# Performance work log

Hardware: AMD Instinct MI355X
Metric: run time of the kernel (lower is better)

The kernel has to match this reference:

```python
import jax, jax.numpy as jnp
import numpy as np

B, T, V, C, H, HS, L, DFF = 8192, 8, 65, 512, 8, 64, 6, 2048
LN_EPS = 1e-5


def _layernorm(x, g, b):
    mu = jnp.mean(x, axis=-1, keepdims=True)
    var = jnp.mean(jnp.square(x - mu), axis=-1, keepdims=True)
    return (x - mu) * jax.lax.rsqrt(var + LN_EPS) * g + b


def setup_inputs() -> dict:
    key = jax.random.key(0)
    ks = jax.random.split(key, 16)
    s = 0.02
    inp = {
        "idx": jax.random.randint(ks[0], (B, T), 0, V),
        "tok_table": jax.random.normal(ks[1], (V, C), jnp.float32) * s,
        "pos_table": jax.random.normal(ks[2], (T, C), jnp.float32) * s,
        "wq": jax.random.normal(ks[3], (L, H, C, HS), jnp.float32) * s,
        "wk": jax.random.normal(ks[4], (L, H, C, HS), jnp.float32) * s,
        "wv": jax.random.normal(ks[5], (L, H, C, HS), jnp.float32) * s,
        "proj_w": jax.random.normal(ks[6], (L, C, C), jnp.float32) * s,
        "proj_b": jnp.zeros((L, C), jnp.float32),
        "w1": jax.random.normal(ks[7], (L, C, DFF), jnp.float32) * s,
        "b1": jnp.zeros((L, DFF), jnp.float32),
        "w2": jax.random.normal(ks[8], (L, DFF, C), jnp.float32) * s,
        "b2": jnp.zeros((L, C), jnp.float32),
        "ln1_g": jnp.ones((L, C), jnp.float32),
        "ln1_b": jnp.zeros((L, C), jnp.float32),
        "ln2_g": jnp.ones((L, C), jnp.float32),
        "ln2_b": jnp.zeros((L, C), jnp.float32),
        "lm_w": jax.random.normal(ks[9], (C, V), jnp.float32) * s,
        "lm_b": jnp.zeros((V,), jnp.float32),
    }
    return inp


def reference(idx, tok_table, pos_table, wq, wk, wv, proj_w, proj_b,
              w1, b1, w2, b2, ln1_g, ln1_b, ln2_g, ln2_b, lm_w, lm_b):
    idx = idx[:, -T:]
    x = tok_table[idx] + pos_table[None, :T, :]  # [B,T,C]
    mask = jnp.tril(jnp.ones((T, T), bool))
    scale = C ** (-0.5)  # NOTE: original scales by n_embed, not head_size
    for l in range(L):
        q = jnp.einsum('btc,hcd->bhtd', x, wq[l])
        k = jnp.einsum('btc,hcd->bhtd', x, wk[l])
        v = jnp.einsum('btc,hcd->bhtd', x, wv[l])
        att = jnp.einsum('bhtd,bhsd->bhts', q, k) * scale
        att = jnp.where(mask, att, -jnp.inf)
        att = jax.nn.softmax(att, axis=-1)
        o = jnp.einsum('bhts,bhsd->bhtd', att, v)
        o = o.transpose(0, 2, 1, 3).reshape(x.shape[0], T, C)  # concat heads
        o = o @ proj_w[l] + proj_b[l]
        x = _layernorm(x + o, ln1_g[l], ln1_b[l])  # post-norm
        h = jax.nn.relu(x @ w1[l] + b1[l]) @ w2[l] + b2[l]
        x = _layernorm(x + h, ln2_g[l], ln2_b[l])
    logits = x @ lm_w + lm_b  # [B,T,V]
    return logits
```

## Files before the change

### kernel.cpp

```cpp
#include <hip/hip_runtime.h>
#include <hip/hip_bf16.h>
#include <math.h>

#define NTOK  65536
#define CDIM  512
#define NHEAD 8
#define HSZ   64
#define NLAYER 6
#define DFF   2048
#define VOCAB 65

typedef unsigned short u16;
typedef __attribute__((ext_vector_type(8))) __bf16 bf16x8;
typedef __attribute__((ext_vector_type(4))) float f32x4;
typedef __attribute__((ext_vector_type(8))) unsigned short ushort8;

__device__ __forceinline__ float b2f(u16 u) {
    union { unsigned int i; float f; } x; x.i = ((unsigned int)u) << 16; return x.f;
}
__device__ __forceinline__ u16 f2b(float f) {
    union { float f; unsigned int i; } x; x.f = f;
    unsigned int r = x.i + 0x7fffu + ((x.i >> 16) & 1u);
    return (u16)(r >> 16);
}

__device__ __forceinline__ void async16(const u16* g, u16* l) {
    __builtin_amdgcn_global_load_lds(
        (const __attribute__((address_space(1))) void*)g,
        (__attribute__((address_space(3))) void*)l, 16, 0, 0);
}

template<int JB, int IB>
__device__ __forceinline__ void mfma_quad(f32x4 (&acc)[4][8],
                                          const bf16x8 (&af)[4][2],
                                          const bf16x8 (&bf)[4][2])
{
#pragma unroll
    for (int kk = 0; kk < 2; kk++)
#pragma unroll
        for (int j = 0; j < 2; j++)
#pragma unroll
            for (int i = 0; i < 4; i++)
                acc[JB + j][IB + i] = __builtin_amdgcn_mfma_f32_16x16x32_bf16(
                    bf[JB + j][kk], af[i][kk], acc[JB + j][IB + i], 0, 0, 0);
}

template<int EPI>
__global__ __launch_bounds__(512, 2)
void gemm256(const u16* __restrict__ A, const u16* __restrict__ Bt,
             void* Cout, const float* __restrict__ bias,
             const u16* res, int K, int lda, int N, int tpb)
{
    extern __shared__ __attribute__((aligned(16))) u16 lds[];
    const int tid = threadIdx.x;
    const int bid = blockIdx.x;

    const int per_x = gridDim.x >> 4;
    const int xcd = bid & 7, wblk = bid >> 3;
    const int mt = xcd * per_x + (wblk >> 1);
    const int q  = wblk & 1;
    const int m0 = mt * 256;
    const int nt0 = q * tpb;

    const int lane = tid & 63, wvv = tid >> 6;
    const int wvm = wvv >> 2, wvn = wvv & 3;
    const int r16 = lane & 15, quad = lane >> 4;
    const int gk0 = quad ^ (r16 & 7);
    const int g0x8 = gk0 * 8, g1x8 = (gk0 ^ 4) * 8;
    const int arow = wvm * 128 + r16;
    const int brow = wvn * 64 + r16;

    const int srow = tid >> 3;
    const int sg = (tid & 7) ^ (srow & 7);
    const u16* pA  = A  + (size_t)(m0 + srow) * lda + sg * 8;
    const u16* pB0 = Bt + (size_t)(nt0 * 256 + srow) * K + sg * 8;
    u16* const ldst = lds + tid * 8;
    const size_t ldaq = (size_t)64 * lda, ldah = (size_t)128 * lda;
    const size_t kq = (size_t)64 * K, kh = (size_t)128 * K;
    const size_t bstride = (size_t)256 * K;

    const int nk = K >> 6;

    f32x4 acc[4][8];
    bf16x8 af[4][2], bf[4][2];

#define STAGE_A(c, kt, h) do { \
    async16(pA + ((h) ? ldah : 0) + (size_t)((kt) * 64),        ldst + (c) * 32768 + (h) * 8192); \
    async16(pA + ((h) ? ldah : 0) + ldaq + (size_t)((kt) * 64), ldst + (c) * 32768 + (h) * 8192 + 4096); } while (0)
#define STAGE_B(c, pb, kt, h) do { \
    async16((pb) + ((h) ? kh : 0) + (size_t)((kt) * 64),        ldst + (c) * 32768 + 16384 + (h) * 8192); \
    async16((pb) + ((h) ? kh : 0) + kq + (size_t)((kt) * 64),   ldst + (c) * 32768 + 16384 + (h) * 8192 + 4096); } while (0)
#define LD_A4(IB0) do { _Pragma("unroll") \
    for (int i = 0; i < 4; i++) { \
        const int ro = cb + (arow + ((IB0) + i) * 16) * 64; \
        af[i][0] = *(const bf16x8*)(const void*)&lds[ro + g0x8]; \
        af[i][1] = *(const bf16x8*)(const void*)&lds[ro + g1x8]; \
    } } while (0)
#define LD_B2(JB0) do { _Pragma("unroll") \
    for (int j = 0; j < 2; j++) { \
        const int ro = cb + 16384 + (brow + ((JB0) + j) * 16) * 64; \
        bf[(JB0) + j][0] = *(const bf16x8*)(const void*)&lds[ro + g0x8]; \
        bf[(JB0) + j][1] = *(const bf16x8*)(const void*)&lds[ro + g1x8]; \
    } } while (0)
#define LGKM0() do { asm volatile("s_waitcnt lgkmcnt(0)" ::: "memory"); \
                     __builtin_amdgcn_sched_barrier(0); } while (0)

    STAGE_A(0, 0, 0); STAGE_A(0, 0, 1);
    STAGE_B(0, pB0, 0, 0); STAGE_B(0, pB0, 0, 1);
    if (nk > 1) {
        STAGE_B(1, pB0, 1, 0); STAGE_B(1, pB0, 1, 1);
        asm volatile("s_waitcnt vmcnt(4)" ::: "memory");
    } else {
        asm volatile("s_waitcnt vmcnt(0)" ::: "memory");
    }
    __builtin_amdgcn_s_barrier();

    for (int j = 0; j < tpb; ++j) {
#pragma unroll
        for (int jj = 0; jj < 4; jj++)
#pragma unroll
            for (int ii = 0; ii < 8; ii++)
                acc[jj][ii] = (f32x4){0.f, 0.f, 0.f, 0.f};

        for (int t = 0; t < nk; ++t) {
            const int c = t & 1;
            const int cb = c * 32768;
            const bool haveA = !((j == tpb - 1) && (t == nk - 1));
            const int kta = (t + 1 < nk) ? (t + 1) : 0;
            int t2 = t + 2, j2 = j;
            if (t2 >= nk) { t2 -= nk; j2++; }
            const bool haveB = (j2 < tpb);
            const u16* pB2 = pB0 + (size_t)j2 * bstride;

            LD_A4(0);
            LD_B2(0);
            if (haveA) STAGE_A(c ^ 1, kta, 0);
            __builtin_amdgcn_s_barrier();
            LGKM0();
            __builtin_amdgcn_s_setprio(1);
            mfma_quad<0, 0>(acc, af, bf);
            __builtin_amdgcn_s_setprio(0);
            __builtin_amdgcn_s_barrier();

            LD_B2(2);
            if (haveA) STAGE_A(c ^ 1, kta, 1);
            __builtin_amdgcn_s_barrier();
            LGKM0();
            __builtin_amdgcn_s_setprio(1);
            mfma_quad<2, 0>(acc, af, bf);
            __builtin_amdgcn_s_setprio(0);
            __builtin_amdgcn_s_barrier();

            LD_A4(4);
            if (haveB) STAGE_B(c, pB2, t2, 0);
            __builtin_amdgcn_s_barrier();
            LGKM0();
            __builtin_amdgcn_s_setprio(1);
            mfma_quad<0, 4>(acc, af, bf);
            __builtin_amdgcn_s_setprio(0);
            __builtin_amdgcn_s_barrier();

            if (haveB) {
                STAGE_B(c, pB2, t2, 1);
                asm volatile("s_waitcnt vmcnt(4)" ::: "memory");
            } else {
                asm volatile("s_waitcnt vmcnt(0)" ::: "memory");
            }
            __builtin_amdgcn_s_barrier();
            __builtin_amdgcn_s_setprio(1);
            mfma_quad<2, 4>(acc, af, bf);
            __builtin_amdgcn_s_setprio(0);
            __builtin_amdgcn_s_barrier();
        }

        const int n0 = (nt0 + j) * 256;
#pragma unroll
        for (int i = 0; i < 8; i++) {
            const int row = m0 + wvm * 128 + i * 16 + r16;
#pragma unroll
            for (int jc = 0; jc < 4; jc++) {
                const int colb = n0 + wvn * 64 + jc * 16 + quad * 4;
                float v[4];
#pragma unroll
                for (int r = 0; r < 4; r++) v[r] = acc[jc][i][r];
                if (EPI == 1 || EPI == 2) {
                    const f32x4 b4 = *(const f32x4*)(const void*)&bias[colb];
#pragma unroll
                    for (int r = 0; r < 4; r++) v[r] += b4[r];
                }
                if (EPI == 1) {
                    const uint2 rv = *(const uint2*)(const void*)&res[(size_t)row * N + colb];
                    v[0] += b2f((u16)(rv.x & 0xffffu));
                    v[1] += b2f((u16)(rv.x >> 16));
                    v[2] += b2f((u16)(rv.y & 0xffffu));
                    v[3] += b2f((u16)(rv.y >> 16));
                }
                if (EPI == 2) {
#pragma unroll
                    for (int r = 0; r < 4; r++) v[r] = fmaxf(v[r], 0.f);
                }
                uint2 o;
                o.x = (unsigned)f2b(v[0]) | ((unsigned)f2b(v[1]) << 16);
                o.y = (unsigned)f2b(v[2]) | ((unsigned)f2b(v[3]) << 16);
                *(uint2*)(void*)&((u16*)Cout)[(size_t)row * N + colb] = o;
            }
        }
    }
#undef STAGE_A
#undef STAGE_B
#undef LD_A4
#undef LD_B2
#undef LGKM0
}

template<int EPI>
__global__ __launch_bounds__(512)
void gemm_bt(const u16* __restrict__ A, const u16* __restrict__ Bt,
             void* __restrict__ Cout, const float* __restrict__ bias,
             const u16* __restrict__ res, int K, int lda, int N, int Nout)
{
    __shared__ u16 lA[2 * 256 * 32];
    __shared__ u16 lB[2 * 128 * 32];
    const int tid  = threadIdx.x;

    const int Nx = gridDim.x;
    const int id = blockIdx.y * Nx + blockIdx.x;
    const int xcd = id & 7;
    const int j0  = id >> 3;
    const int mt  = xcd + 8 * (j0 / Nx);
    const int nt  = j0 - (j0 / Nx) * Nx;
    const int m0  = mt * 256;
    const int n0  = nt * 128;

    const int lane = tid & 63;
    const int wv   = tid >> 6;
    const int wr   = (wv >> 1) * 64;
    const int wc   = (wv & 1) * 64;
    const int r16  = lane & 15;
    const int quad = lane >> 4;

    f32x4 acc[4][4] = {};

    const int srow = tid >> 2, skseg = (tid & 3) * 8;
    const u16* pA  = A  + (size_t)(m0 + srow) * lda + skseg;
    const u16* pA2 = pA + (size_t)128 * lda;
    const u16* pB  = Bt + (size_t)(n0 + srow) * K + skseg;
    u16* lAt = &lA[(size_t)tid * 8];
    u16* lBt = &lB[(size_t)tid * 8];

    for (int k0 = 0; k0 < K; k0 += 64) {
        async16(pA  + k0,      lAt);
        async16(pA2 + k0,      lAt + 4096);
        async16(pA  + k0 + 32, lAt + 8192);
        async16(pA2 + k0 + 32, lAt + 12288);
        async16(pB  + k0,      lBt);
        async16(pB  + k0 + 32, lBt + 4096);
        __syncthreads();

#pragma unroll
        for (int s = 0; s < 2; s++) {
            const u16* bA = &lA[s * 8192];
            const u16* bB = &lB[s * 4096];
            bf16x8 af[4], bfr[4];
#pragma unroll
            for (int i = 0; i < 4; i++)
                af[i] = *(const bf16x8*)(const void*)&bA[(wr + i * 16 + r16) * 32 + quad * 8];
#pragma unroll
            for (int j = 0; j < 4; j++)
                bfr[j] = *(const bf16x8*)(const void*)&bB[(wc + j * 16 + r16) * 32 + quad * 8];
#pragma unroll
            for (int j = 0; j < 4; j++)
#pragma unroll
                for (int i = 0; i < 4; i++)
                    acc[j][i] = __builtin_amdgcn_mfma_f32_16x16x32_bf16(bfr[j], af[i], acc[j][i], 0, 0, 0);
        }
        __syncthreads();
    }

#pragma unroll
    for (int i = 0; i < 4; i++) {
        const int row = m0 + wr + i * 16 + r16;
#pragma unroll
        for (int j = 0; j < 4; j++) {
            const int colb = n0 + wc + j * 16 + quad * 4;
            float v[4];
#pragma unroll
            for (int r = 0; r < 4; r++) v[r] = acc[j][i][r];
            if (EPI == 3) {
#pragma unroll
                for (int r = 0; r < 4; r++) {
                    const int col = colb + r;
                    if (col < Nout)
                        ((float*)Cout)[(size_t)row * Nout + col] = v[r] + bias[col];
                }
            } else {
                uint2 o;
                o.x = (unsigned)f2b(v[0]) | ((unsigned)f2b(v[1]) << 16);
                o.y = (unsigned)f2b(v[2]) | ((unsigned)f2b(v[3]) << 16);
                *(uint2*)(void*)&((u16*)Cout)[(size_t)row * N + colb] = o;
            }
        }
    }
}

__global__ __launch_bounds__(256)
void attn_k(u16* __restrict__ qkv)
{
    __shared__ float sq[4][8][65], sk[4][8][65], sv[4][8][65], sp[4][64];
    const int w = threadIdx.x >> 6, lane = threadIdx.x & 63;
    const int unit = blockIdx.x * 4 + w;
    const int b = unit >> 3, h = unit & 7;
    const size_t base = (size_t)b * 8 * 1536 + h * 64;
    {
        const int t = lane >> 3, d0 = (lane & 7) * 8;
        const ushort8 q8 = *(const ushort8*)(const void*)&qkv[base + t * 1536 + d0];
        const ushort8 k8 = *(const ushort8*)(const void*)&qkv[base + t * 1536 + 512 + d0];
        const ushort8 v8 = *(const ushort8*)(const void*)&qkv[base + t * 1536 + 1024 + d0];
#pragma unroll
        for (int i = 0; i < 8; i++) {
            sq[w][t][d0 + i] = b2f(q8[i]);
            sk[w][t][d0 + i] = b2f(k8[i]);
            sv[w][t][d0 + i] = b2f(v8[i]);
        }
    }
    __syncthreads();
    const int t = lane >> 3, s = lane & 7;
    float sc = -1e30f;
    if (s <= t) {
        float d = 0.f;
#pragma unroll
        for (int c = 0; c < 64; c++) d += sq[w][t][c] * sk[w][s][c];
        sc = d * 0.04419417382415922f;
    }
    float mx = sc;
#pragma unroll
    for (int m = 1; m < 8; m <<= 1) mx = fmaxf(mx, __shfl_xor(mx, m, 8));
    float e = __expf(sc - mx);
    if (s > t) e = 0.f;
    float sum = e;
#pragma unroll
    for (int m = 1; m < 8; m <<= 1) sum += __shfl_xor(sum, m, 8);
    sp[w][lane] = e / sum;
    __syncthreads();
    {
        const int tt = lane >> 3, d0 = (lane & 7) * 8;
        float a[8] = {};
#pragma unroll
        for (int ss = 0; ss < 8; ss++) {
            const float p = sp[w][tt * 8 + ss];
#pragma unroll
            for (int i = 0; i < 8; i++) a[i] += p * sv[w][ss][d0 + i];
        }
        ushort8 o;
#pragma unroll
        for (int i = 0; i < 8; i++) o[i] = f2b(a[i]);
        *(ushort8*)(void*)&qkv[base + tt * 1536 + d0] = o;
    }
}

__global__ __launch_bounds__(256)
void ln_k(const u16* __restrict__ y, const float* __restrict__ g,
          const float* __restrict__ be, u16* __restrict__ x)
{
    const int w = threadIdx.x >> 6, lane = threadIdx.x & 63;
    const size_t tok = (size_t)blockIdx.x * 4 + w;
    const u16* row = y + tok * 512 + lane * 8;
    ushort8 raw = *(const ushort8*)(const void*)row;
    float v[8];
#pragma unroll
    for (int i = 0; i < 8; i++) v[i] = b2f(raw[i]);
    float s = 0.f;
#pragma unroll
    for (int i = 0; i < 8; i++) s += v[i];
#pragma unroll
    for (int m = 1; m < 64; m <<= 1) s += __shfl_xor(s, m, 64);
    const float mu = s * (1.f / 512.f);
    float q = 0.f;
#pragma unroll
    for (int i = 0; i < 8; i++) { float d = v[i] - mu; q += d * d; }
#pragma unroll
    for (int m = 1; m < 64; m <<= 1) q += __shfl_xor(q, m, 64);
    const float inv = rsqrtf(q * (1.f / 512.f) + 1e-5f);
    f32x4 g0  = *(const f32x4*)(const void*)&g[lane * 8];
    f32x4 g1  = *(const f32x4*)(const void*)&g[lane * 8 + 4];
    f32x4 b0  = *(const f32x4*)(const void*)&be[lane * 8];
    f32x4 b1v = *(const f32x4*)(const void*)&be[lane * 8 + 4];
    ushort8 o;
#pragma unroll
    for (int i = 0; i < 4; i++) o[i]     = f2b((v[i] - mu) * inv * g0[i] + b0[i]);
#pragma unroll
    for (int i = 0; i < 4; i++) o[i + 4] = f2b((v[i + 4] - mu) * inv * g1[i] + b1v[i]);
    *(ushort8*)(void*)&x[tok * 512 + lane * 8] = o;
}

__global__ __launch_bounds__(256)
void embed_k(const int* __restrict__ idx, const float* __restrict__ tokt,
             const float* __restrict__ pos, u16* __restrict__ xb)
{
    const int gid = blockIdx.x * 256 + threadIdx.x;
    const int tk = gid >> 6, seg = (gid & 63) * 8;
    const int t = tk & 7;
    const int ix = idx[tk];
    const f32x4 a0 = *(const f32x4*)(const void*)&tokt[(size_t)ix * 512 + seg];
    const f32x4 a1 = *(const f32x4*)(const void*)&tokt[(size_t)ix * 512 + seg + 4];
    const f32x4 p0 = *(const f32x4*)(const void*)&pos[t * 512 + seg];
    const f32x4 p1 = *(const f32x4*)(const void*)&pos[t * 512 + seg + 4];
    ushort8 o;
#pragma unroll
    for (int i = 0; i < 4; i++) o[i]     = f2b(a0[i] + p0[i]);
#pragma unroll
    for (int i = 0; i < 4; i++) o[i + 4] = f2b(a1[i] + p1[i]);
    *(ushort8*)(void*)&xb[(size_t)tk * 512 + seg] = o;
}

__global__ __launch_bounds__(256)
void conv_t2_k(const float* __restrict__ in, u16* __restrict__ out, int K, int N)
{
    __shared__ float t[32][33];
    const int tx = threadIdx.x & 31, ty4 = (threadIdx.x >> 5) * 4;
    const int n0 = blockIdx.x * 32, k0 = blockIdx.y * 32, l = blockIdx.z;
    const size_t per = (size_t)K * N;
    const float* src = in + l * per;
#pragma unroll
    for (int r = 0; r < 4; r++)
        t[ty4 + r][tx] = src[(size_t)(k0 + ty4 + r) * N + n0 + tx];
    __syncthreads();
    u16* dst = out + l * per;
#pragma unroll
    for (int r = 0; r < 4; r++)
        dst[(size_t)(n0 + ty4 + r) * K + k0 + tx] = f2b(t[tx][ty4 + r]);
}

__global__ __launch_bounds__(256)
void conv_qkv2_k(const float* __restrict__ wq, const float* __restrict__ wk,
                 const float* __restrict__ wv, u16* __restrict__ out)
{
    __shared__ float t[32][33];
    const int tx = threadIdx.x & 31, ty4 = (threadIdx.x >> 5) * 4;
    const int c0 = blockIdx.x * 32, d0 = blockIdx.y * 32;
    const int z = blockIdx.z;
    const int sel = z / 48, rem = z - sel * 48;
    const int l = rem >> 3, h = rem & 7;
    const float* src = (sel == 0) ? wq : (sel == 1) ? wk : wv;
    const float* sb = src + (((size_t)l * 8 + h) * 512) * 64;
#pragma unroll
    for (int r = 0; r < 4; r++)
        t[ty4 + r][tx] = sb[(size_t)(c0 + ty4 + r) * 64 + d0 + tx];
    __syncthreads();
    u16* dst = out + (size_t)l * 786432 + (size_t)(sel * 512 + h * 64 + d0) * 512;
#pragma unroll
    for (int r = 0; r < 4; r++)
        dst[(size_t)(ty4 + r) * 512 + c0 + tx] = f2b(t[tx][ty4 + r]);
}

__global__ __launch_bounds__(256)
void conv_lm_k(const float* __restrict__ lm_w, u16* __restrict__ out)
{
    int gid = blockIdx.x * 256 + threadIdx.x;
    int n = gid >> 9, c = gid & 511;
    out[gid] = (n < VOCAB) ? f2b(lm_w[(size_t)c * VOCAB + n]) : (u16)0;
}

extern "C" void kernel_launch(void* const* d_in, const int* in_sizes, int n_in,
                              void* d_out, int out_size, void* d_ws, size_t ws_size,
                              hipStream_t stream)
{
    const int*   idx    = (const int*)  d_in[0];
    const float* tokt   = (const float*)d_in[1];
    const float* post   = (const float*)d_in[2];
    const float* wq     = (const float*)d_in[3];
    const float* wk     = (const float*)d_in[4];
    const float* wvp    = (const float*)d_in[5];
    const float* proj_w = (const float*)d_in[6];
    const float* proj_b = (const float*)d_in[7];
    const float* w1     = (const float*)d_in[8];
    const float* b1     = (const float*)d_in[9];
    const float* w2     = (const float*)d_in[10];
    const float* b2     = (const float*)d_in[11];
    const float* ln1_g  = (const float*)d_in[12];
    const float* ln1_b  = (const float*)d_in[13];
    const float* ln2_g  = (const float*)d_in[14];
    const float* ln2_b  = (const float*)d_in[15];
    const float* lm_w   = (const float*)d_in[16];
    const float* lm_b   = (const float*)d_in[17];
    float* out = (float*)d_out;

    static int smem_set = 0;
    if (!smem_set) {
        smem_set = 1;
        hipFuncSetAttribute(reinterpret_cast<const void*>(&gemm256<0>),
                            hipFuncAttributeMaxDynamicSharedMemorySize, 131072);
        hipFuncSetAttribute(reinterpret_cast<const void*>(&gemm256<1>),
                            hipFuncAttributeMaxDynamicSharedMemorySize, 131072);
        hipFuncSetAttribute(reinterpret_cast<const void*>(&gemm256<2>),
                            hipFuncAttributeMaxDynamicSharedMemorySize, 131072);
    }

    char* ws = (char*)d_ws;
    u16* wqkvt = (u16*)(ws + 0);
    u16* wprjt = (u16*)(ws + 9437184);
    u16* ww1t  = (u16*)(ws + 12582912);
    u16* ww2t  = (u16*)(ws + 25165824);
    u16* wlmt  = (u16*)(ws + 37748736);
    u16* xb    = (u16*)(ws + 37879808);
    char* big  = ws + 104988672;

    const size_t fixed_bytes = 104988672ull;
    const size_t avail = (ws_size > fixed_bytes) ? (ws_size - fixed_bytes) : 0;
    int chunk_a = 8192, chunk_m = 8192;
    const int cands[3] = {65536, 32768, 16384};
    for (int i = 0; i < 3; i++)
        if ((size_t)cands[i] * 3072ull <= avail) { chunk_a = cands[i]; break; }
    for (int i = 0; i < 3; i++)
        if ((size_t)cands[i] * 4096ull <= avail) { chunk_m = cands[i]; break; }
    const int nca = NTOK / chunk_a, ncm = NTOK / chunk_m;
    u16* qkvc = (u16*)big;
    u16* h1c  = (u16*)big;

    conv_qkv2_k<<<dim3(16, 2, 144), 256, 0, stream>>>(wq, wk, wvp, wqkvt);
    conv_t2_k  <<<dim3(16, 16, 6), 256, 0, stream>>>(proj_w, wprjt, 512, 512);
    conv_t2_k  <<<dim3(64, 16, 6), 256, 0, stream>>>(w1, ww1t, 512, 2048);
    conv_t2_k  <<<dim3(16, 64, 6), 256, 0, stream>>>(w2, ww2t, 2048, 512);
    conv_lm_k  <<<128 * 512 / 256, 256, 0, stream>>>(lm_w, wlmt);

    embed_k<<<NTOK * 64 / 256, 256, 0, stream>>>(idx, tokt, post, xb);

    for (int l = 0; l < NLAYER; l++) {
        for (int c = 0; c < nca; c++) {
            const size_t t0 = (size_t)c * chunk_a;
            const int grid = (chunk_a / 256) * 2;
            gemm256<0><<<dim3(grid), 512, 131072, stream>>>(
                xb + t0 * 512, wqkvt + (size_t)l * 786432, qkvc,
                nullptr, nullptr, 512, 512, 1536, 3);
            attn_k<<<chunk_a / 4, 256, 0, stream>>>(qkvc);
            gemm256<1><<<dim3(grid), 512, 131072, stream>>>(
                qkvc, wprjt + (size_t)l * 262144, xb + t0 * 512,
                proj_b + l * 512, xb + t0 * 512, 512, 1536, 512, 1);
        }
        ln_k<<<NTOK / 4, 256, 0, stream>>>(xb, ln1_g + l * 512, ln1_b + l * 512, xb);
        for (int c = 0; c < ncm; c++) {
            const size_t t0 = (size_t)c * chunk_m;
            const int grid = (chunk_m / 256) * 2;
            gemm256<2><<<dim3(grid), 512, 131072, stream>>>(
                xb + t0 * 512, ww1t + (size_t)l * 1048576, h1c,
                b1 + l * 2048, nullptr, 512, 512, 2048, 4);
            gemm256<1><<<dim3(grid), 512, 131072, stream>>>(
                h1c, ww2t + (size_t)l * 1048576, xb + t0 * 512,
                b2 + l * 512, xb + t0 * 512, 2048, 2048, 512, 1);
        }
        ln_k<<<NTOK / 4, 256, 0, stream>>>(xb, ln2_g + l * 512, ln2_b + l * 512, xb);
    }

    gemm_bt<3><<<dim3(1, 256), 512, 0, stream>>>(
        xb, wlmt, out, lm_b, nullptr, 512, 512, 128, VOCAB);
}
```

Measured before the change: 4.151 ms.

## Specialize GEMM dimensions as template constants and simplify to single-barrier double buffering

The GEMM kernel now takes K, LDA, N and tiles-per-block as template parameters, so strides and trip counts are compile-time constants and the k-loop can be unrolled. The hand-interleaved four-phase schedule is replaced by a plain double buffer. That schedule split A/B staging across sub-steps, prefetched B two tiles ahead and used several barriers with lgkmcnt waits. The new loop issues all next-tile async loads up front, runs all MFMAs, then waits vmcnt(0) and takes one barrier. This removes barrier and wait overhead per k-step, but it shortens the prefetch distance and hides less memory latency behind compute.

Measured after the change: 5.257 ms. 26.7% more time.

```diff
diff --git a/kernel.cpp b/kernel.cpp
--- a/kernel.cpp
+++ b/kernel.cpp
@@ -45,13 +45,14 @@
                     bf[JB + j][kk], af[i][kk], acc[JB + j][IB + i], 0, 0, 0);
 }
 
-template<int EPI>
+template<int EPI, int K, int LDA, int N, int TPB>
 __global__ __launch_bounds__(512, 2)
 void gemm256(const u16* __restrict__ A, const u16* __restrict__ Bt,
-             void* Cout, const float* __restrict__ bias,
-             const u16* res, int K, int lda, int N, int tpb)
+             void* Cout, const float* __restrict__ bias, const u16* res)
 {
     extern __shared__ __attribute__((aligned(16))) u16 lds[];
+    constexpr int NK = K >> 6;
+    constexpr size_t BSTRIDE = (size_t)256 * K;
     const int tid = threadIdx.x;
     const int bid = blockIdx.x;
 
@@ -60,7 +61,7 @@
     const int mt = xcd * per_x + (wblk >> 1);
     const int q  = wblk & 1;
     const int m0 = mt * 256;
-    const int nt0 = q * tpb;
+    const int nt0 = q * TPB;
 
     const int lane = tid & 63, wvv = tid >> 6;
     const int wvm = wvv >> 2, wvn = wvv & 3;
@@ -72,14 +73,11 @@
 
     const int srow = tid >> 3;
     const int sg = (tid & 7) ^ (srow & 7);
-    const u16* pA  = A  + (size_t)(m0 + srow) * lda + sg * 8;
+    const u16* pA  = A  + (size_t)(m0 + srow) * LDA + sg * 8;
     const u16* pB0 = Bt + (size_t)(nt0 * 256 + srow) * K + sg * 8;
     u16* const ldst = lds + tid * 8;
-    const size_t ldaq = (size_t)64 * lda, ldah = (size_t)128 * lda;
-    const size_t kq = (size_t)64 * K, kh = (size_t)128 * K;
-    const size_t bstride = (size_t)256 * K;
-
-    const int nk = K >> 6;
+    constexpr size_t ldaq = (size_t)64 * LDA, ldah = (size_t)128 * LDA;
+    constexpr size_t kq = (size_t)64 * K, kh = (size_t)128 * K;
 
     f32x4 acc[4][8];
     bf16x8 af[4][2], bf[4][2];
@@ -102,74 +100,42 @@
         bf[(JB0) + j][0] = *(const bf16x8*)(const void*)&lds[ro + g0x8]; \
         bf[(JB0) + j][1] = *(const bf16x8*)(const void*)&lds[ro + g1x8]; \
     } } while (0)
-#define LGKM0() do { asm volatile("s_waitcnt lgkmcnt(0)" ::: "memory"); \
-                     __builtin_amdgcn_sched_barrier(0); } while (0)
 
     STAGE_A(0, 0, 0); STAGE_A(0, 0, 1);
     STAGE_B(0, pB0, 0, 0); STAGE_B(0, pB0, 0, 1);
-    if (nk > 1) {
-        STAGE_B(1, pB0, 1, 0); STAGE_B(1, pB0, 1, 1);
-        asm volatile("s_waitcnt vmcnt(4)" ::: "memory");
-    } else {
-        asm volatile("s_waitcnt vmcnt(0)" ::: "memory");
-    }
+    asm volatile("s_waitcnt vmcnt(0)" ::: "memory");
     __builtin_amdgcn_s_barrier();
 
-    for (int j = 0; j < tpb; ++j) {
+    for (int j = 0; j < TPB; ++j) {
+        const u16* pBj = pB0 + (size_t)j * BSTRIDE;
 #pragma unroll
         for (int jj = 0; jj < 4; jj++)
 #pragma unroll
             for (int ii = 0; ii < 8; ii++)
                 acc[jj][ii] = (f32x4){0.f, 0.f, 0.f, 0.f};
 
-        for (int t = 0; t < nk; ++t) {
+#pragma unroll 4
+        for (int t = 0; t < NK; ++t) {
             const int c = t & 1;
             const int cb = c * 32768;
-            const bool haveA = !((j == tpb - 1) && (t == nk - 1));
-            const int kta = (t + 1 < nk) ? (t + 1) : 0;
-            int t2 = t + 2, j2 = j;
-            if (t2 >= nk) { t2 -= nk; j2++; }
-            const bool haveB = (j2 < tpb);
-            const u16* pB2 = pB0 + (size_t)j2 * bstride;
-
-            LD_A4(0);
-            LD_B2(0);
-            if (haveA) STAGE_A(c ^ 1, kta, 0);
-            __builtin_amdgcn_s_barrier();
-            LGKM0();
+            if (t + 1 < NK) {
+                STAGE_A(c ^ 1, t + 1, 0); STAGE_A(c ^ 1, t + 1, 1);
+                STAGE_B(c ^ 1, pBj, t + 1, 0); STAGE_B(c ^ 1, pBj, t + 1, 1);
+            } else if (j + 1 < TPB) {
+                STAGE_A(c ^ 1, 0, 0); STAGE_A(c ^ 1, 0, 1);
+                STAGE_B(c ^ 1, pBj + BSTRIDE, 0, 0); STAGE_B(c ^ 1, pBj + BSTRIDE, 0, 1);
+            }
+            LD_A4(0); LD_B2(0); LD_B2(2);
             __builtin_amdgcn_s_setprio(1);
             mfma_quad<0, 0>(acc, af, bf);
-            __builtin_amdgcn_s_setprio(0);
-            __builtin_amdgcn_s_barrier();
-
-            LD_B2(2);
-            if (haveA) STAGE_A(c ^ 1, kta, 1);
-            __builtin_amdgcn_s_barrier();
-            LGKM0();
-            __builtin_amdgcn_s_setprio(1);
             mfma_quad<2, 0>(acc, af, bf);
             __builtin_amdgcn_s_setprio(0);
-            __builtin_amdgcn_s_barrier();
-
             LD_A4(4);
-            if (haveB) STAGE_B(c, pB2, t2, 0);
-            __builtin_amdgcn_s_barrier();
-            LGKM0();
             __builtin_amdgcn_s_setprio(1);
             mfma_quad<0, 4>(acc, af, bf);
-            __builtin_amdgcn_s_setprio(0);
-            __builtin_amdgcn_s_barrier();
-
-            if (haveB) {
-                STAGE_B(c, pB2, t2, 1);
-                asm volatile("s_waitcnt vmcnt(4)" ::: "memory");
-            } else {
-                asm volatile("s_waitcnt vmcnt(0)" ::: "memory");
-            }
-            __builtin_amdgcn_s_barrier();
-            __builtin_amdgcn_s_setprio(1);
             mfma_quad<2, 4>(acc, af, bf);
             __builtin_amdgcn_s_setprio(0);
+            asm volatile("s_waitcnt vmcnt(0)" ::: "memory");
             __builtin_amdgcn_s_barrier();
         }
 
@@ -210,7 +176,6 @@
 #undef STAGE_B
 #undef LD_A4
 #undef LD_B2
-#undef LGKM0
 }
 
 template<int EPI>
@@ -488,11 +453,13 @@
     static int smem_set = 0;
     if (!smem_set) {
         smem_set = 1;
-        hipFuncSetAttribute(reinterpret_cast<const void*>(&gemm256<0>),
+        hipFuncSetAttribute(reinterpret_cast<const void*>(&gemm256<0, 512, 512, 1536, 3>),
                             hipFuncAttributeMaxDynamicSharedMemorySize, 131072);
-        hipFuncSetAttribute(reinterpret_cast<const void*>(&gemm256<1>),
+        hipFuncSetAttribute(reinterpret_cast<const void*>(&gemm256<1, 512, 1536, 512, 1>),
                             hipFuncAttributeMaxDynamicSharedMemorySize, 131072);
-        hipFuncSetAttribute(reinterpret_cast<const void*>(&gemm256<2>),
+        hipFuncSetAttribute(reinterpret_cast<const void*>(&gemm256<2, 512, 512, 2048, 4>),
+                            hipFuncAttributeMaxDynamicSharedMemorySize, 131072);
+        hipFuncSetAttribute(reinterpret_cast<const void*>(&gemm256<1, 2048, 2048, 512, 1>),
                             hipFuncAttributeMaxDynamicSharedMemorySize, 131072);
     }
 
@@ -529,24 +496,23 @@
         for (int c = 0; c < nca; c++) {
             const size_t t0 = (size_t)c * chunk_a;
             const int grid = (chunk_a / 256) * 2;
-            gemm256<0><<<dim3(grid), 512, 131072, stream>>>(
-                xb + t0 * 512, wqkvt + (size_t)l * 786432, qkvc,
-                nullptr, nullptr, 512, 512, 1536, 3);
+            gemm256<0, 512, 512, 1536, 3><<<dim3(grid), 512, 131072, stream>>>(
+                xb + t0 * 512, wqkvt + (size_t)l * 786432, qkvc, nullptr, nullptr);
             attn_k<<<chunk_a / 4, 256, 0, stream>>>(qkvc);
-            gemm256<1><<<dim3(grid), 512, 131072, stream>>>(
+            gemm256<1, 512, 1536, 512, 1><<<dim3(grid), 512, 131072, stream>>>(
                 qkvc, wprjt + (size_t)l * 262144, xb + t0 * 512,
-                proj_b + l * 512, xb + t0 * 512, 512, 1536, 512, 1);
+                proj_b + l * 512, xb + t0 * 512);
         }
         ln_k<<<NTOK / 4, 256, 0, stream>>>(xb, ln1_g + l * 512, ln1_b + l * 512, xb);
         for (int c = 0; c < ncm; c++) {
             const size_t t0 = (size_t)c * chunk_m;
             const int grid = (chunk_m / 256) * 2;
-            gemm256<2><<<dim3(grid), 512, 131072, stream>>>(
+            gemm256<2, 512, 512, 2048, 4><<<dim3(grid), 512, 131072, stream>>>(
                 xb + t0 * 512, ww1t + (size_t)l * 1048576, h1c,
-                b1 + l * 2048, nullptr, 512, 512, 2048, 4);
-            gemm256<1><<<dim3(grid), 512, 131072, stream>>>(
+                b1 + l * 2048, nullptr);
+            gemm256<1, 2048, 2048, 512, 1><<<dim3(grid), 512, 131072, stream>>>(
                 h1c, ww2t + (size_t)l * 1048576, xb + t0 * 512,
-                b2 + l * 512, xb + t0 * 512, 2048, 2048, 512, 1);
+                b2 + l * 512, xb + t0 * 512);
         }
         ln_k<<<NTOK / 4, 256, 0, stream>>>(xb, ln2_g + l * 512, ln2_b + l * 512, xb);
     }
```
